# Optimization experiments

Measured on AMD Instinct MI355X. Metric: run time of the kernel, lower is better.

The kernel has to match this reference:

```python
import jax, jax.numpy as jnp
import numpy as np
import math

HEADS = 2
DH = 64
INNER = HEADS * DH  # 128
TOPK = 128
ALPHA = 10.0
N_FREQ = 8  # feature_dim // (2*input_dim) = 64 // 8
OMEGAS = jnp.logspace(1.0, math.log10(128.0), N_FREQ)           # sigma_q = 128
OMEGAS_L = [jnp.logspace(1.0, math.log10(s), N_FREQ) for s in (128.0, 32.0)]
LAYER_NUM = 2


def calc_gamma(grid, omegas):
    # grid: (Q, 4) -> (Q, 4*2*n_freq)
    arg = jnp.pi * grid[:, :, None] * omegas[None, None, :]      # (Q,4,n)
    g = jnp.concatenate([jnp.sin(arg), jnp.cos(arg)], axis=-1)   # (Q,4,2n)
    return g.reshape(grid.shape[0], -1)


def setup_inputs() -> dict:
    key = jax.random.key(0)
    ks = jax.random.split(key, 20)
    B, Q, L, HD, FD, OD = 2, 4096, 1024, 256, 64, 1

    def w(k, shape, fan_in):
        return jax.random.normal(k, shape, dtype=jnp.float32) * (1.0 / np.sqrt(fan_in))

    inp = {
        'x': jax.random.uniform(ks[0], (B, Q, 4), dtype=jnp.float32),
        'tokens': jax.random.normal(ks[1], (B, L, HD), dtype=jnp.float32),
        'query_W': w(ks[2], (FD, HD), FD),
        'query_b': jnp.zeros((HD,), jnp.float32),
        'q_W': w(ks[3], (HD, INNER), HD),
        'kv_W': w(ks[4], (HD, 2 * INNER), HD),
        'out_W': w(ks[5], (INNER, HD), INNER),
        'out_b': jnp.zeros((HD,), jnp.float32),
        'band_W': w(ks[6], (LAYER_NUM, FD, HD), FD),
        'band_b': jnp.zeros((LAYER_NUM, HD), jnp.float32),
        'mod_W': w(ks[7], (LAYER_NUM, HD, HD), HD),
        'mod_b': jnp.zeros((LAYER_NUM, HD), jnp.float32),
        'hv_W': w(ks[8], (LAYER_NUM - 1, HD, HD), HD),
        'hv_b': jnp.zeros((LAYER_NUM - 1, HD), jnp.float32),
        'outl_W': w(ks[9], (LAYER_NUM, HD, OD), HD),
        'outl_b': jnp.zeros((LAYER_NUM, OD), jnp.float32),
        'gD': 8, 'gH': 8, 'gW': 8, 'gT': 8,
    }
    return inp


def reference(x, tokens, query_W, query_b, q_W, kv_W, out_W, out_b,
              band_W, band_b, mod_W, mod_b, hv_W, hv_b, outl_W, outl_b,
              gD, gH, gW, gT):
    B, Q, _ = x.shape
    L = tokens.shape[1]
    grid = x[0]  # (Q, 4) — torch code uses x[0] for all batches

    # --- patch index + approximate relative distances -> sparse attn indices ---
    z_i = (grid[:, 0] * gD).astype(jnp.int32)
    y_i = (grid[:, 1] * gH).astype(jnp.int32)
    x_i = (grid[:, 2] * gW).astype(jnp.int32)
    t_i = (grid[:, 3] * gT).astype(jnp.int32)
    idx = ((t_i * gD + z_i) * gH + y_i) * gW + x_i               # (Q,)
    N = gD * gH * gW * gT
    t = idx / N                                                  # (Q,) float
    tok_pos = (jnp.arange(L, dtype=jnp.float32) + 0.5) / L       # (L,)
    bias = ALPHA * (t[:, None] - tok_pos[None, :]) ** 2          # (Q, L)
    # top-k SMALLEST distances (identical across batch, compute once)
    _, attn_idx = jax.lax.top_k(-bias, TOPK)                     # (Q, k)

    # --- query features ---
    gamma_q = calc_gamma(grid, OMEGAS)                           # (Q, 64)
    x_q = jax.nn.relu(gamma_q @ query_W + query_b)               # (Q, 256)
    x_q = jnp.broadcast_to(x_q[None], (B, Q, x_q.shape[-1]))

    # --- sparse shared-token cross attention ---
    scale = DH ** -0.5
    q = (x_q @ q_W).reshape(B, Q, HEADS, DH)                     # (B,Q,H,Dh)
    kv = tokens @ kv_W                                           # (B,L,2*inner)
    k_full, v_full = kv[..., :INNER], kv[..., INNER:]            # (B,L,inner)
    k_sp = k_full[:, attn_idx, :].reshape(B, Q, TOPK, HEADS, DH)  # (B,Q,k,H,Dh)
    v_sp = v_full[:, attn_idx, :].reshape(B, Q, TOPK, HEADS, DH)
    sim = jnp.einsum('bqhd,bqkhd->bhqk', q, k_sp) * scale        # (B,H,Q,k)
    attn = jax.nn.softmax(sim, axis=-1)
    o = jnp.einsum('bhqk,bqkhd->bqhd', attn, v_sp).reshape(B, Q, INNER)
    modulation = o @ out_W + out_b                               # (B,Q,256)

    # --- per-band modulation ---
    mods = []
    for l in range(LAYER_NUM):
        gamma_l = calc_gamma(grid, OMEGAS_L[l])                  # (Q, 64)
        h_l = jax.nn.relu(gamma_l @ band_W[l] + band_b[l])       # (Q, 256)
        m_l = jax.nn.relu(h_l[None] + modulation @ mod_W[l] + mod_b[l])
        mods.append(m_l)

    h_v = [mods[0]]
    for i in range(LAYER_NUM - 1):
        h_v.append(jax.nn.relu((mods[i + 1] + h_v[i]) @ hv_W[i] + hv_b[i]))

    out = sum(h_v[i] @ outl_W[i] + outl_b[i] for i in range(LAYER_NUM))
    return out  # (B, Q, output_dim)
```

## Files before the change

### kernel.cpp

```cpp
#include <hip/hip_runtime.h>
#include <math.h>

#define BN     2
#define QN     4096
#define LN     1024
#define TOPKN  128
#define PI_F   3.14159265358979323846f

#define LOG2R0 0.52543879f
#define LOG2R1 0.23972456f

#define NCMAX  320
#define PFP    332

typedef __attribute__((ext_vector_type(8))) short  s16x8;
typedef __attribute__((ext_vector_type(4))) short  s16x4;
typedef __attribute__((ext_vector_type(4))) float  f32x4;
typedef unsigned short u16;

__device__ __forceinline__ u16 f2bf(float f) {
    unsigned int u = __float_as_uint(f);
    u = (u + 0x7FFFu + ((u >> 16) & 1u)) >> 16;
    return (u16)u;
}

__device__ __forceinline__ size_t wtile(int n, int k, int K) {
    return (size_t)((n >> 4) * (K >> 5) + (k >> 5)) * 512 + (n & 15) * 32 + (k & 31);
}
__device__ __forceinline__ size_t kidx(int b, int l, int d) {
    return (((size_t)(b * 64 + (l >> 4)) * 16 + (d >> 3)) * 16 + (l & 15)) * 8 + (d & 7);
}
__device__ __forceinline__ size_t vidx(int b, int n, int k) {
    return (((size_t)(b * 8 + (n >> 4)) * 128 + (k >> 3)) * 16 + (n & 15)) * 8 + (k & 7);
}

struct KvS { u16 tok[32 * 264]; u16 stage[256 * 40]; float vtile[128][40]; };
struct QS  { float shx[128]; u16 gam[32 * 72]; u16 xq[32 * 264]; u16 stage[256 * 40]; };
struct TrS { float tile[8][32][33]; };
struct SoS { int hist[1024]; int cur[1024]; };
union PrepS { KvS kv; QS q; TrS tr; SoS so; };

__global__ __launch_bounds__(1024) void prep_kernel(
    const float* __restrict__ tokens, const float* __restrict__ kv_W,
    const float* __restrict__ x, const float* __restrict__ query_W,
    const float* __restrict__ query_b, const float* __restrict__ q_W,
    const float* __restrict__ outW, const float* __restrict__ bandW,
    const float* __restrict__ modW, const float* __restrict__ hvW,
    const int* __restrict__ gDp, const int* __restrict__ gHp,
    const int* __restrict__ gWp, const int* __restrict__ gTp,
    u16* __restrict__ qall, u16* __restrict__ kbf, u16* __restrict__ vtbf,
    u16* __restrict__ outT, u16* __restrict__ bandT,
    u16* __restrict__ modT, u16* __restrict__ hvT,
    int* __restrict__ perm, int* __restrict__ ssort)
{
    __shared__ __align__(16) PrepS sm;
    const int bid = blockIdx.x;
    const int t   = threadIdx.x;
    const int wid = t >> 6, lane = t & 63;
    const int quad = lane >> 4, l16 = lane & 15;

    if (bid < 64) {
        int l0 = bid * 32;
        int b = l0 >> 10, lloc = l0 & 1023;
        #pragma unroll
        for (int i = 0; i < 8; i++) {
            int idx = i * 1024 + t; int row = idx >> 8, col = idx & 255;
            sm.kv.tok[row * 264 + col] = f2bf(tokens[(size_t)(l0 + row) * 256 + col]);
        }
        int m0 = (wid & 1) * 16;
        int c0 = (wid >> 1) * 32;
        f32x4 acc[2];
        acc[0] = (f32x4){0.f, 0.f, 0.f, 0.f};
        acc[1] = (f32x4){0.f, 0.f, 0.f, 0.f};
        for (int kc = 0; kc < 8; kc++) {
            __syncthreads();
            #pragma unroll
            for (int i = 0; i < 8; i++) {
                int idx = i * 1024 + t; int k = idx >> 8, n = idx & 255;
                sm.kv.stage[n * 40 + k] = f2bf(kv_W[(size_t)(kc * 32 + k) * 256 + n]);
            }
            __syncthreads();
            s16x8 a = *(const s16x8*)&sm.kv.tok[(m0 + l16) * 264 + kc * 32 + quad * 8];
            #pragma unroll
            for (int sub = 0; sub < 2; sub++) {
                s16x8 bfr = *(const s16x8*)&sm.kv.stage[(c0 + sub * 16 + l16) * 40 + quad * 8];
                acc[sub] = __builtin_amdgcn_mfma_f32_16x16x32_bf16(a, bfr, acc[sub], 0, 0, 0);
            }
        }
        #pragma unroll
        for (int sub = 0; sub < 2; sub++) {
            int col = c0 + sub * 16 + l16;
            if (col < 128) {
                #pragma unroll
                for (int r = 0; r < 4; r++) {
                    int lg = l0 + m0 + quad * 4 + r;
                    kbf[kidx(lg >> 10, lg & 1023, col)] = f2bf(acc[sub][r]);
                }
            } else {
                #pragma unroll
                for (int r = 0; r < 4; r++)
                    sm.kv.vtile[col - 128][m0 + quad * 4 + r] = acc[sub][r];
            }
        }
        __syncthreads();
        {
            int col = t >> 3, rg = (t & 7) * 4;
            float4 v4 = *(const float4*)&sm.kv.vtile[col][rg];
            s16x4 pk;
            pk[0] = (short)f2bf(v4.x); pk[1] = (short)f2bf(v4.y);
            pk[2] = (short)f2bf(v4.z); pk[3] = (short)f2bf(v4.w);
            *(s16x4*)&vtbf[vidx(b, col, lloc + rg)] = pk;
        }
    } else if (bid < 192) {
        int p0 = (bid - 64) * 32;
        if (t < 128) sm.q.shx[t] = x[p0 * 4 + t];
        __syncthreads();
        #pragma unroll
        for (int j = 0; j < 2; j++) {
            int e = t * 2 + j;
            int g = e >> 6, f = e & 63;
            int c = f >> 4, jj = f & 15, oi = jj & 7;
            float om = 10.0f * exp2f((float)oi * LOG2R0);
            float arg = PI_F * sm.q.shx[g * 4 + c] * om;
            sm.q.gam[g * 72 + f] = f2bf((jj < 8) ? __sinf(arg) : __cosf(arg));
        }
        int m0 = (wid & 1) * 16;
        {
            int c0 = (wid >> 1) * 32;
            f32x4 acc[2];
            acc[0] = (f32x4){0.f, 0.f, 0.f, 0.f};
            acc[1] = (f32x4){0.f, 0.f, 0.f, 0.f};
            for (int kc = 0; kc < 2; kc++) {
                __syncthreads();
                #pragma unroll
                for (int i = 0; i < 8; i++) {
                    int idx = i * 1024 + t; int k = idx >> 8, n = idx & 255;
                    sm.q.stage[n * 40 + k] = f2bf(query_W[(size_t)(kc * 32 + k) * 256 + n]);
                }
                __syncthreads();
                s16x8 a = *(const s16x8*)&sm.q.gam[(m0 + l16) * 72 + kc * 32 + quad * 8];
                #pragma unroll
                for (int sub = 0; sub < 2; sub++) {
                    s16x8 bfr = *(const s16x8*)&sm.q.stage[(c0 + sub * 16 + l16) * 40 + quad * 8];
                    acc[sub] = __builtin_amdgcn_mfma_f32_16x16x32_bf16(a, bfr, acc[sub], 0, 0, 0);
                }
            }
            #pragma unroll
            for (int sub = 0; sub < 2; sub++) {
                int col = c0 + sub * 16 + l16;
                float bias = query_b[col];
                #pragma unroll
                for (int r = 0; r < 4; r++)
                    sm.q.xq[(m0 + quad * 4 + r) * 264 + col] = f2bf(fmaxf(acc[sub][r] + bias, 0.f));
            }
        }
        {
            int n0q = (wid >> 1) * 16;
            f32x4 acc2 = (f32x4){0.f, 0.f, 0.f, 0.f};
            for (int kc = 0; kc < 8; kc++) {
                __syncthreads();
                #pragma unroll
                for (int i = 0; i < 4; i++) {
                    int idx = i * 1024 + t; int k = idx >> 7, n = idx & 127;
                    sm.q.stage[n * 40 + k] = f2bf(q_W[(size_t)(kc * 32 + k) * 128 + n]);
                }
                __syncthreads();
                s16x8 a = *(const s16x8*)&sm.q.xq[(m0 + l16) * 264 + kc * 32 + quad * 8];
                s16x8 bfr = *(const s16x8*)&sm.q.stage[(n0q + l16) * 40 + quad * 8];
                acc2 = __builtin_amdgcn_mfma_f32_16x16x32_bf16(a, bfr, acc2, 0, 0, 0);
            }
            #pragma unroll
            for (int r = 0; r < 4; r++)
                qall[(size_t)(p0 + m0 + quad * 4 + r) * 128 + n0q + l16] = f2bf(acc2[r]);
        }
    } else if (bid < 224) {
        int base = (bid - 192) * 8;
        int tx = t & 31, ty = (t >> 5) & 31;
        #pragma unroll
        for (int it = 0; it < 8; it++) {
            int lt_g = base + it;
            const float* src; int K, lt;
            if (lt_g < 32)       { src = outW;  K = 128; lt = lt_g; }
            else if (lt_g < 64)  { src = bandW; K = 128; lt = lt_g - 32; }
            else if (lt_g < 192) { src = modW;  K = 512; lt = lt_g - 64; }
            else                 { src = hvW;   K = 256; lt = lt_g - 192; }
            int tk = K >> 5;
            int k0 = (lt % tk) * 32, n0 = (lt / tk) * 32;
            sm.tr.tile[it][ty][tx] = src[(size_t)(k0 + ty) * 256 + n0 + tx];
        }
        __syncthreads();
        #pragma unroll
        for (int it = 0; it < 8; it++) {
            int lt_g = base + it;
            u16* dst; int K, lt;
            if (lt_g < 32)       { dst = outT;  K = 128; lt = lt_g; }
            else if (lt_g < 64)  { dst = bandT; K = 128; lt = lt_g - 32; }
            else if (lt_g < 192) { dst = modT;  K = 512; lt = lt_g - 64; }
            else                 { dst = hvT;   K = 256; lt = lt_g - 192; }
            int tk = K >> 5;
            int k0 = (lt % tk) * 32, n0 = (lt / tk) * 32;
            dst[wtile(n0 + ty, k0 + tx, K)] = f2bf(sm.tr.tile[it][tx][ty]);
        }
    } else {
        int gD = gDp[0], gH = gHp[0], gW = gWp[0], gT = gTp[0];
        int Ng = gD * gH * gW * gT;
        sm.so.hist[t] = 0;
        __syncthreads();
        int sarr[4];
        #pragma unroll
        for (int i = 0; i < 4; i++) {
            int q = i * 1024 + t;
            float4 xv = *(const float4*)&x[q * 4];
            int zi = (int)(xv.x * (float)gD);
            int yi = (int)(xv.y * (float)gH);
            int xi = (int)(xv.z * (float)gW);
            int ti = (int)(xv.w * (float)gT);
            int idx = ((ti * gD + zi) * gH + yi) * gW + xi;
            float tt = (float)idx / (float)Ng;
            int s = (int)ceilf(tt * (float)LN - ((float)(TOPKN / 2) + 0.5f));
            s = min(max(s, 0), LN - TOPKN);
            sarr[i] = s;
            atomicAdd(&sm.so.hist[s], 1);
        }
        __syncthreads();
        int cnt = sm.so.hist[t];
        int incl = cnt;
        #pragma unroll
        for (int off = 1; off < 64; off <<= 1) {
            int u = __shfl_up(incl, off);
            if (lane >= off) incl += u;
        }
        if (lane == 63) sm.so.cur[wid] = incl;
        __syncthreads();
        if (wid == 0) {
            int v = (lane < 16) ? sm.so.cur[lane] : 0;
            #pragma unroll
            for (int off = 1; off < 16; off <<= 1) {
                int u = __shfl_up(v, off);
                if (lane >= off) v += u;
            }
            if (lane < 16) sm.so.cur[lane] = v;
        }
        __syncthreads();
        int woff = wid ? sm.so.cur[wid - 1] : 0;
        sm.so.hist[t] = woff + incl - cnt;
        __syncthreads();
        #pragma unroll
        for (int i = 0; i < 4; i++) {
            int q = i * 1024 + t;
            int pos = atomicAdd(&sm.so.hist[sarr[i]], 1);
            perm[pos] = q;
            ssort[pos] = sarr[i];
        }
    }
}

__global__ __launch_bounds__(1024, 8) void fused_kernel(
    const float* __restrict__ x,
    const u16* __restrict__ kbf, const u16* __restrict__ vtbf,
    const u16* __restrict__ qall,
    const int* __restrict__ perm, const int* __restrict__ ssort,
    const u16* __restrict__ outT, const float* __restrict__ out_b,
    const u16* __restrict__ bandT, const float* __restrict__ band_b,
    const u16* __restrict__ modT, const float* __restrict__ mod_b,
    const u16* __restrict__ hvT, const float* __restrict__ hv_b,
    const float* __restrict__ outl_W, const float* __restrict__ outl_b,
    float* __restrict__ out)
{
    const int bid = blockIdx.x;
    const int b   = bid >> 8;
    const int sp0 = (bid & 255) * 16;
    const int t   = threadIdx.x;
    const int wid = t >> 6, lane = t & 63;
    const int quad = lane >> 4, l16 = lane & 15;

    __shared__ __align__(16) u16 q_bf[16 * 136];
    __shared__ __align__(16) u16 gam_lds[32 * 72];
    __shared__ __align__(16) float scores32[32 * PFP];
    __shared__ __align__(16) u16 o_lds[16 * 136];
    __shared__ float fin[256];
    __shared__ float sh_xc[64];
    __shared__ int sh_pq[16], sh_s[16];

    u16* modu_lds = (u16*)scores32;
    u16* s01_lds  = ((u16*)scores32) + 16 * 264;

    if (t < 16) { sh_pq[t] = perm[sp0 + t]; sh_s[t] = ssort[sp0 + t]; }
    __syncthreads();

    {
        int m = t >> 6, d = (t & 63) * 2;
        *(unsigned int*)&q_bf[m * 136 + d] =
            *(const unsigned int*)&qall[(size_t)sh_pq[m] * 128 + d];
    }
    if (t < 64) sh_xc[t] = x[(size_t)sh_pq[t >> 2] * 4 + (t & 3)];
    __syncthreads();

    #pragma unroll
    for (int j = 0; j < 2; j++) {
        int e = t * 2 + j;
        int l = e >> 10, g = (e >> 6) & 15, f = e & 63;
        int c = f >> 4, jj = f & 15, oi = jj & 7;
        float om = 10.0f * exp2f((float)oi * (l ? LOG2R1 : LOG2R0));
        float arg = PI_F * sh_xc[g * 4 + c] * om;
        gam_lds[(l * 16 + g) * 72 + f] = f2bf((jj < 8) ? __sinf(arg) : __cosf(arg));
    }

    const int u0    = sh_s[0] & ~15;
    const int ncols = min((sh_s[15] + 128 - u0 + 31) & ~31, NCMAX);
    const int nsub  = ncols >> 4;
    const int nkc   = ncols >> 5;

    {
        s16x8 aq00 = *(const s16x8*)&q_bf[l16 * 136 + quad * 8];
        s16x8 aq01 = *(const s16x8*)&q_bf[l16 * 136 + 32 + quad * 8];
        s16x8 aq10 = *(const s16x8*)&q_bf[l16 * 136 + 64 + quad * 8];
        s16x8 aq11 = *(const s16x8*)&q_bf[l16 * 136 + 96 + quad * 8];
        for (int j = wid; j < 2 * nsub; j += 16) {
            int h = (j >= nsub) ? 1 : 0;
            int sub = j - h * nsub;
            int lrow = u0 + sub * 16 + l16;
            f32x4 acc = (f32x4){0.f, 0.f, 0.f, 0.f};
            s16x8 b0 = *(const s16x8*)&kbf[kidx(b, lrow, h * 64 + quad * 8)];
            s16x8 b1 = *(const s16x8*)&kbf[kidx(b, lrow, h * 64 + 32 + quad * 8)];
            acc = __builtin_amdgcn_mfma_f32_16x16x32_bf16(h ? aq10 : aq00, b0, acc, 0, 0, 0);
            acc = __builtin_amdgcn_mfma_f32_16x16x32_bf16(h ? aq11 : aq01, b1, acc, 0, 0, 0);
            #pragma unroll
            for (int r = 0; r < 4; r++)
                scores32[(h * 16 + quad * 4 + r) * PFP + sub * 16 + l16] = acc[r];
        }
    }
    __syncthreads();

    {
        int g = wid;
        int sg = sh_s[g];
        #pragma unroll
        for (int rr = 0; rr < 2; rr++) {
            int row = g + rr * 16;
            float vals[5]; int ok[5];
            float mx = -1e30f;
            #pragma unroll
            for (int i = 0; i < 5; i++) {
                int c = lane + 64 * i;
                float v = scores32[row * PFP + c] * 0.125f;
                int key = u0 + c;
                int o2 = (c < ncols) && (key >= sg) && (key < sg + 128);
                vals[i] = v; ok[i] = o2;
                if (o2) mx = fmaxf(mx, v);
            }
            #pragma unroll
            for (int off = 1; off < 64; off <<= 1) mx = fmaxf(mx, __shfl_xor(mx, off));
            float sum = 0.f, e5[5];
            #pragma unroll
            for (int i = 0; i < 5; i++) {
                float e = ok[i] ? __expf(vals[i] - mx) : 0.f;
                e5[i] = e; sum += e;
            }
            #pragma unroll
            for (int off = 1; off < 64; off <<= 1) sum += __shfl_xor(sum, off);
            float inv = 1.f / sum;
            u16* prow = (u16*)&scores32[row * PFP];
            #pragma unroll
            for (int i = 0; i < 5; i++) {
                int c = lane + 64 * i;
                if (c < ncols) prow[c] = f2bf(e5[i] * inv);
            }
        }
    }
    __syncthreads();

    if (wid < 8) {
        int n0 = wid * 16;
        int hh = n0 >> 6;
        const u16* prow = (const u16*)&scores32[(hh * 16 + l16) * PFP];
        f32x4 acc = (f32x4){0.f, 0.f, 0.f, 0.f};
        for (int kc = 0; kc < nkc; kc++) {
            s16x8 a = *(const s16x8*)&prow[kc * 32 + quad * 8];
            int koff = u0 + kc * 32 + quad * 8;
            koff = min(koff, 1016);
            s16x8 bfr = *(const s16x8*)&vtbf[vidx(b, n0 + l16, koff)];
            acc = __builtin_amdgcn_mfma_f32_16x16x32_bf16(a, bfr, acc, 0, 0, 0);
        }
        #pragma unroll
        for (int r = 0; r < 4; r++)
            o_lds[(quad * 4 + r) * 136 + n0 + l16] = f2bf(acc[r]);
    }
    __syncthreads();

    const int n0 = wid * 16;
    float m0f[4];

    {
        f32x4 acc = (f32x4){0.f, 0.f, 0.f, 0.f};
        #pragma unroll
        for (int kc = 0; kc < 4; kc++) {
            s16x8 a = *(const s16x8*)&o_lds[l16 * 136 + kc * 32 + quad * 8];
            s16x8 bfr = *(const s16x8*)&outT[wtile(n0 + l16, kc * 32 + quad * 8, 128)];
            acc = __builtin_amdgcn_mfma_f32_16x16x32_bf16(a, bfr, acc, 0, 0, 0);
        }
        int col = n0 + l16;
        float bias = out_b[col];
        #pragma unroll
        for (int r = 0; r < 4; r++)
            modu_lds[(quad * 4 + r) * 264 + col] = f2bf(acc[r] + bias);
    }
    __syncthreads();

    #pragma unroll
    for (int l = 0; l < 2; l++) {
        f32x4 acc1 = (f32x4){0.f, 0.f, 0.f, 0.f};
        f32x4 acc2 = (f32x4){0.f, 0.f, 0.f, 0.f};
        #pragma unroll
        for (int kc = 0; kc < 2; kc++) {
            s16x8 a = *(const s16x8*)&gam_lds[(l * 16 + l16) * 72 + kc * 32 + quad * 8];
            s16x8 bfr = *(const s16x8*)&bandT[wtile(n0 + l16, l * 64 + kc * 32 + quad * 8, 128)];
            acc1 = __builtin_amdgcn_mfma_f32_16x16x32_bf16(a, bfr, acc1, 0, 0, 0);
        }
        #pragma unroll
        for (int kc = 0; kc < 8; kc++) {
            s16x8 a = *(const s16x8*)&modu_lds[l16 * 264 + kc * 32 + quad * 8];
            s16x8 bfr = *(const s16x8*)&modT[wtile(n0 + l16, l * 256 + kc * 32 + quad * 8, 512)];
            acc2 = __builtin_amdgcn_mfma_f32_16x16x32_bf16(a, bfr, acc2, 0, 0, 0);
        }
        int col = n0 + l16;
        float bb = band_b[l * 256 + col];
        float mb = mod_b[l * 256 + col];
        #pragma unroll
        for (int r = 0; r < 4; r++) {
            float hval = fmaxf(acc1[r] + bb, 0.f);
            float mval = fmaxf(hval + acc2[r] + mb, 0.f);
            if (l == 0) m0f[r] = mval;
            else s01_lds[(quad * 4 + r) * 264 + col] = f2bf(m0f[r] + mval);
        }
    }
    __syncthreads();

    {
        f32x4 acc = (f32x4){0.f, 0.f, 0.f, 0.f};
        #pragma unroll
        for (int kc = 0; kc < 8; kc++) {
            s16x8 a = *(const s16x8*)&s01_lds[l16 * 264 + kc * 32 + quad * 8];
            s16x8 bfr = *(const s16x8*)&hvT[wtile(n0 + l16, kc * 32 + quad * 8, 256)];
            acc = __builtin_amdgcn_mfma_f32_16x16x32_bf16(a, bfr, acc, 0, 0, 0);
        }
        int col = n0 + l16;
        float w0 = outl_W[col], w1 = outl_W[256 + col], hb = hv_b[col];
        #pragma unroll
        for (int r = 0; r < 4; r++) {
            float hvv = fmaxf(acc[r] + hb, 0.f);
            float pv = m0f[r] * w0 + hvv * w1;
            #pragma unroll
            for (int off = 1; off < 16; off <<= 1) pv += __shfl_xor(pv, off);
            if (l16 == 0) fin[wid * 16 + quad * 4 + r] = pv;
        }
    }
    __syncthreads();
    if (t < 16) {
        float s2 = outl_b[0] + outl_b[1];
        #pragma unroll
        for (int w = 0; w < 16; w++) s2 += fin[w * 16 + t];
        out[(size_t)b * QN + sh_pq[t]] = s2;
    }
}

extern "C" void kernel_launch(void* const* d_in, const int* in_sizes, int n_in,
                              void* d_out, int out_size, void* d_ws, size_t ws_size,
                              hipStream_t stream)
{
    const float* x       = (const float*)d_in[0];
    const float* tokens  = (const float*)d_in[1];
    const float* query_W = (const float*)d_in[2];
    const float* query_b = (const float*)d_in[3];
    const float* q_W     = (const float*)d_in[4];
    const float* kv_W    = (const float*)d_in[5];
    const float* out_W   = (const float*)d_in[6];
    const float* out_b   = (const float*)d_in[7];
    const float* band_W  = (const float*)d_in[8];
    const float* band_b  = (const float*)d_in[9];
    const float* mod_W   = (const float*)d_in[10];
    const float* mod_b   = (const float*)d_in[11];
    const float* hv_W    = (const float*)d_in[12];
    const float* hv_b    = (const float*)d_in[13];
    const float* outl_W  = (const float*)d_in[14];
    const float* outl_b  = (const float*)d_in[15];
    const int*   gD      = (const int*)d_in[16];
    const int*   gH      = (const int*)d_in[17];
    const int*   gW      = (const int*)d_in[18];
    const int*   gT      = (const int*)d_in[19];

    float* ws   = (float*)d_ws;
    u16* qall   = (u16*)ws;
    u16* wb = (u16*)(ws + 524288);
    u16* kbf   = wb;
    u16* vtbf  = wb + 262144;
    u16* outT  = wb + 524288;
    u16* bandT = wb + 557056;
    u16* modT  = wb + 589824;
    u16* hvT   = wb + 720896;
    int* perm  = (int*)(wb + 786432);
    int* ssort = perm + 4096;
    float* out = (float*)d_out;

    prep_kernel<<<225, 1024, 0, stream>>>(tokens, kv_W, x, query_W, query_b, q_W,
                                          out_W, band_W, mod_W, hv_W,
                                          gD, gH, gW, gT,
                                          qall, kbf, vtbf, outT, bandT, modT, hvT,
                                          perm, ssort);
    fused_kernel<<<512, 1024, 0, stream>>>(x, kbf, vtbf, qall, perm, ssort,
        outT, out_b, bandT, band_b, modT, mod_b, hvT, hv_b,
        outl_W, outl_b, out);
}
```

Baseline: 125.8 us.

## Load GEMM weight fragments directly from global memory, skipping LDS staging

In the prep kernel, the kv, query and q projection GEMMs no longer stage weight tiles through shared memory with barriers each k-chunk. Each lane now gathers its B fragment straight from global memory with strided loads and converts it to bf16. V is written to its transposed bf16 layout directly from the accumulators instead of going through an LDS tile. In the attention kernel, the PV loop now runs a fixed NCMAX/32 iterations and the probability row is written unconditionally, which removes data-dependent bounds but can do extra MFMA work on zero probabilities.

```diff
diff --git a/kernel.cpp b/kernel.cpp
--- a/kernel.cpp
+++ b/kernel.cpp
@@ -24,6 +24,13 @@
     return (u16)u;
 }
 
+__device__ __forceinline__ s16x8 ldB(const float* __restrict__ base, int stride) {
+    s16x8 r;
+    #pragma unroll
+    for (int jj = 0; jj < 8; jj++) r[jj] = (short)f2bf(base[(size_t)jj * stride]);
+    return r;
+}
+
 __device__ __forceinline__ size_t wtile(int n, int k, int K) {
     return (size_t)((n >> 4) * (K >> 5) + (k >> 5)) * 512 + (n & 15) * 32 + (k & 31);
 }
@@ -34,8 +41,8 @@
     return (((size_t)(b * 8 + (n >> 4)) * 128 + (k >> 3)) * 16 + (n & 15)) * 8 + (k & 7);
 }
 
-struct KvS { u16 tok[32 * 264]; u16 stage[256 * 40]; float vtile[128][40]; };
-struct QS  { float shx[128]; u16 gam[32 * 72]; u16 xq[32 * 264]; u16 stage[256 * 40]; };
+struct KvS { u16 tok[32 * 264]; };
+struct QS  { float shx[128]; u16 gam[32 * 72]; u16 xq[32 * 264]; };
 struct TrS { float tile[8][32][33]; };
 struct SoS { int hist[1024]; int cur[1024]; };
 union PrepS { KvS kv; QS q; TrS tr; SoS so; };
@@ -67,23 +74,17 @@
             int idx = i * 1024 + t; int row = idx >> 8, col = idx & 255;
             sm.kv.tok[row * 264 + col] = f2bf(tokens[(size_t)(l0 + row) * 256 + col]);
         }
+        __syncthreads();
         int m0 = (wid & 1) * 16;
         int c0 = (wid >> 1) * 32;
         f32x4 acc[2];
         acc[0] = (f32x4){0.f, 0.f, 0.f, 0.f};
         acc[1] = (f32x4){0.f, 0.f, 0.f, 0.f};
         for (int kc = 0; kc < 8; kc++) {
-            __syncthreads();
-            #pragma unroll
-            for (int i = 0; i < 8; i++) {
-                int idx = i * 1024 + t; int k = idx >> 8, n = idx & 255;
-                sm.kv.stage[n * 40 + k] = f2bf(kv_W[(size_t)(kc * 32 + k) * 256 + n]);
-            }
-            __syncthreads();
             s16x8 a = *(const s16x8*)&sm.kv.tok[(m0 + l16) * 264 + kc * 32 + quad * 8];
             #pragma unroll
             for (int sub = 0; sub < 2; sub++) {
-                s16x8 bfr = *(const s16x8*)&sm.kv.stage[(c0 + sub * 16 + l16) * 40 + quad * 8];
+                s16x8 bfr = ldB(&kv_W[(size_t)(kc * 32 + quad * 8) * 256 + c0 + sub * 16 + l16], 256);
                 acc[sub] = __builtin_amdgcn_mfma_f32_16x16x32_bf16(a, bfr, acc[sub], 0, 0, 0);
             }
         }
@@ -92,24 +93,14 @@
             int col = c0 + sub * 16 + l16;
             if (col < 128) {
                 #pragma unroll
-                for (int r = 0; r < 4; r++) {
-                    int lg = l0 + m0 + quad * 4 + r;
-                    kbf[kidx(lg >> 10, lg & 1023, col)] = f2bf(acc[sub][r]);
-                }
+                for (int r = 0; r < 4; r++)
+                    kbf[kidx(b, lloc + m0 + quad * 4 + r, col)] = f2bf(acc[sub][r]);
             } else {
-                #pragma unroll
-                for (int r = 0; r < 4; r++)
-                    sm.kv.vtile[col - 128][m0 + quad * 4 + r] = acc[sub][r];
-            }
-        }
-        __syncthreads();
-        {
-            int col = t >> 3, rg = (t & 7) * 4;
-            float4 v4 = *(const float4*)&sm.kv.vtile[col][rg];
-            s16x4 pk;
-            pk[0] = (short)f2bf(v4.x); pk[1] = (short)f2bf(v4.y);
-            pk[2] = (short)f2bf(v4.z); pk[3] = (short)f2bf(v4.w);
-            *(s16x4*)&vtbf[vidx(b, col, lloc + rg)] = pk;
+                s16x4 pk;
+                pk[0] = (short)f2bf(acc[sub][0]); pk[1] = (short)f2bf(acc[sub][1]);
+                pk[2] = (short)f2bf(acc[sub][2]); pk[3] = (short)f2bf(acc[sub][3]);
+                *(s16x4*)&vtbf[vidx(b, col - 128, lloc + m0 + quad * 4)] = pk;
+            }
         }
     } else if (bid < 192) {
         int p0 = (bid - 64) * 32;
@@ -124,6 +115,7 @@
             float arg = PI_F * sm.q.shx[g * 4 + c] * om;
             sm.q.gam[g * 72 + f] = f2bf((jj < 8) ? __sinf(arg) : __cosf(arg));
         }
+        __syncthreads();
         int m0 = (wid & 1) * 16;
         {
             int c0 = (wid >> 1) * 32;
@@ -131,17 +123,10 @@
             acc[0] = (f32x4){0.f, 0.f, 0.f, 0.f};
             acc[1] = (f32x4){0.f, 0.f, 0.f, 0.f};
             for (int kc = 0; kc < 2; kc++) {
-                __syncthreads();
-                #pragma unroll
-                for (int i = 0; i < 8; i++) {
-                    int idx = i * 1024 + t; int k = idx >> 8, n = idx & 255;
-                    sm.q.stage[n * 40 + k] = f2bf(query_W[(size_t)(kc * 32 + k) * 256 + n]);
-                }
-                __syncthreads();
                 s16x8 a = *(const s16x8*)&sm.q.gam[(m0 + l16) * 72 + kc * 32 + quad * 8];
                 #pragma unroll
                 for (int sub = 0; sub < 2; sub++) {
-                    s16x8 bfr = *(const s16x8*)&sm.q.stage[(c0 + sub * 16 + l16) * 40 + quad * 8];
+                    s16x8 bfr = ldB(&query_W[(size_t)(kc * 32 + quad * 8) * 256 + c0 + sub * 16 + l16], 256);
                     acc[sub] = __builtin_amdgcn_mfma_f32_16x16x32_bf16(a, bfr, acc[sub], 0, 0, 0);
                 }
             }
@@ -154,19 +139,13 @@
                     sm.q.xq[(m0 + quad * 4 + r) * 264 + col] = f2bf(fmaxf(acc[sub][r] + bias, 0.f));
             }
         }
+        __syncthreads();
         {
             int n0q = (wid >> 1) * 16;
             f32x4 acc2 = (f32x4){0.f, 0.f, 0.f, 0.f};
             for (int kc = 0; kc < 8; kc++) {
-                __syncthreads();
-                #pragma unroll
-                for (int i = 0; i < 4; i++) {
-                    int idx = i * 1024 + t; int k = idx >> 7, n = idx & 127;
-                    sm.q.stage[n * 40 + k] = f2bf(q_W[(size_t)(kc * 32 + k) * 128 + n]);
-                }
-                __syncthreads();
                 s16x8 a = *(const s16x8*)&sm.q.xq[(m0 + l16) * 264 + kc * 32 + quad * 8];
-                s16x8 bfr = *(const s16x8*)&sm.q.stage[(n0q + l16) * 40 + quad * 8];
+                s16x8 bfr = ldB(&q_W[(size_t)(kc * 32 + quad * 8) * 128 + n0q + l16], 128);
                 acc2 = __builtin_amdgcn_mfma_f32_16x16x32_bf16(a, bfr, acc2, 0, 0, 0);
             }
             #pragma unroll
@@ -309,7 +288,6 @@
     const int u0    = sh_s[0] & ~15;
     const int ncols = min((sh_s[15] + 128 - u0 + 31) & ~31, NCMAX);
     const int nsub  = ncols >> 4;
-    const int nkc   = ncols >> 5;
 
     {
         s16x8 aq00 = *(const s16x8*)&q_bf[l16 * 136 + quad * 8];
@@ -364,7 +342,7 @@
             #pragma unroll
             for (int i = 0; i < 5; i++) {
                 int c = lane + 64 * i;
-                if (c < ncols) prow[c] = f2bf(e5[i] * inv);
+                prow[c] = f2bf(e5[i] * inv);
             }
         }
     }
@@ -375,7 +353,7 @@
         int hh = n0 >> 6;
         const u16* prow = (const u16*)&scores32[(hh * 16 + l16) * PFP];
         f32x4 acc = (f32x4){0.f, 0.f, 0.f, 0.f};
-        for (int kc = 0; kc < nkc; kc++) {
+        for (int kc = 0; kc < (NCMAX >> 5); kc++) {
             s16x8 a = *(const s16x8*)&prow[kc * 32 + quad * 8];
             int koff = u0 + kc * 32 + quad * 8;
             koff = min(koff, 1016);
```

Result: no change. 125.0 us (-0.7%).
